# Performance work log

Hardware: AMD Instinct MI355X
Metric: run time of the kernel (lower is better)

## Reference

```python
import jax, jax.numpy as jnp
import numpy as np


def setup_inputs() -> dict:
    key = jax.random.key(0)
    k1, k2 = jax.random.split(key)
    B, N = 2, 8192
    pred = jax.random.normal(k1, (B, N, 3), dtype=jnp.float32)
    gt = jax.random.normal(k2, (B, N, 3), dtype=jnp.float32)
    return {"pred": pred, "gt": gt}


def reference(pred, gt):
    # dist[b, i, j] = ||pred[b, j] - gt[b, i]||_2  (matches torch expand layout:
    # expanded_pred[b,i,j] = pred[b,j], expanded_gt[b,i,j] = gt[b,i]).
    # Computed via the squared-norm expansion to avoid the [B,N,N,3] tensor.
    g2 = jnp.sum(gt * gt, axis=-1)[:, :, None]        # [B, N, 1]
    p2 = jnp.sum(pred * pred, axis=-1)[:, None, :]    # [B, 1, N]
    cross = jnp.einsum('bid,bjd->bij', gt, pred)      # [B, N, N]
    dist = jnp.sqrt(jnp.maximum(g2 + p2 - 2.0 * cross, 0.0))  # [B, N, N]
    dist1 = jnp.min(dist, axis=2)  # min over pred for each gt point
    dist2 = jnp.min(dist, axis=1)  # min over gt for each pred point
    return jnp.mean(jnp.mean(dist1, axis=1) + jnp.mean(dist2, axis=1))
```

## Files before the change

### kernel.cpp

```cpp
#include <hip/hip_runtime.h>
#include <math.h>


#define TILE 1024

__global__ __launch_bounds__(256) void chamfer_partial(
    const float* __restrict__ pred, const float* __restrict__ gt,
    float* __restrict__ ws_max, int N, int B, int S) {
  __shared__ float4 sb[TILE];
  const int tid = threadIdx.x;
  const int z   = blockIdx.z;
  const int dir = z / B;
  const int b   = z - dir * B;
  const float* qbase = (dir == 0) ? gt   : pred;
  const float* obase = (dir == 0) ? pred : gt;

  const int q = blockIdx.x * blockDim.x + tid;
  const float qx = qbase[(size_t)(b * N + q) * 3 + 0];
  const float qy = qbase[(size_t)(b * N + q) * 3 + 1];
  const float qz = qbase[(size_t)(b * N + q) * 3 + 2];

  const int chunk = N / S;
  const int start = blockIdx.y * chunk;

  float m0 = -INFINITY, m1 = -INFINITY, m2 = -INFINITY, m3 = -INFINITY;

  for (int t0 = 0; t0 < chunk; t0 += TILE) {
    for (int p = tid; p < TILE; p += blockDim.x) {
      const float* src = &obase[(size_t)(b * N + start + t0 + p) * 3];
      const float x = src[0], y = src[1], zc = src[2];
      sb[p] = make_float4(x, y, zc, -0.5f * (x * x + y * y + zc * zc));
    }
    __syncthreads();
    #pragma unroll 2
    for (int k = 0; k < TILE; k += 4) {
      const float4 p0 = sb[k + 0];
      const float4 p1 = sb[k + 1];
      const float4 p2 = sb[k + 2];
      const float4 p3 = sb[k + 3];
      m0 = fmaxf(m0, fmaf(qx, p0.x, fmaf(qy, p0.y, fmaf(qz, p0.z, p0.w))));
      m1 = fmaxf(m1, fmaf(qx, p1.x, fmaf(qy, p1.y, fmaf(qz, p1.z, p1.w))));
      m2 = fmaxf(m2, fmaf(qx, p2.x, fmaf(qy, p2.y, fmaf(qz, p2.z, p2.w))));
      m3 = fmaxf(m3, fmaf(qx, p3.x, fmaf(qy, p3.y, fmaf(qz, p3.z, p3.w))));
    }
    __syncthreads();
  }
  const float m = fmaxf(fmaxf(m0, m1), fmaxf(m2, m3));
  ws_max[((size_t)z * N + q) * S + blockIdx.y] = m;
}

__global__ __launch_bounds__(256) void chamfer_combine(
    const float* __restrict__ pred, const float* __restrict__ gt,
    const float* __restrict__ ws_max, float* __restrict__ out,
    int N, int B, int S, float scale) {
  const int idx = blockIdx.x * blockDim.x + threadIdx.x;
  const int z   = idx / N;
  const int q   = idx - z * N;
  const int dir = z / B;
  const int b   = z - dir * B;
  const float* qbase = (dir == 0) ? gt : pred;

  const float qx = qbase[(size_t)(b * N + q) * 3 + 0];
  const float qy = qbase[(size_t)(b * N + q) * 3 + 1];
  const float qz = qbase[(size_t)(b * N + q) * 3 + 2];
  const float g2 = qx * qx + qy * qy + qz * qz;

  const float* wp = &ws_max[((size_t)z * N + q) * S];
  float m = wp[0];
  for (int s = 1; s < S; ++s) m = fmaxf(m, wp[s]);

  float v = sqrtf(fmaxf(g2 - 2.0f * m, 0.0f));

  for (int off = 32; off > 0; off >>= 1) v += __shfl_down(v, off);
  __shared__ float wsum[4];
  const int wid = threadIdx.x >> 6, lane = threadIdx.x & 63;
  if (lane == 0) wsum[wid] = v;
  __syncthreads();
  if (threadIdx.x == 0) {
    const float s4 = wsum[0] + wsum[1] + wsum[2] + wsum[3];
    atomicAdd(out, s4 * scale);
  }
}

extern "C" void kernel_launch(void* const* d_in, const int* in_sizes, int n_in,
                              void* d_out, int out_size, void* d_ws, size_t ws_size,
                              hipStream_t stream) {
  const float* pred = (const float*)d_in[0];
  const float* gt   = (const float*)d_in[1];
  float* out = (float*)d_out;

  const int B = 2;
  const int N = in_sizes[0] / (B * 3);

  int S = 8;
  size_t need = (size_t)2 * B * N * S * sizeof(float);
  while (S > 1 && need > ws_size) { S >>= 1; need >>= 1; }
  float* ws_max = (float*)d_ws;

  hipMemsetAsync(d_out, 0, sizeof(float), stream);

  dim3 g1(N / 256, S, 2 * B);
  chamfer_partial<<<g1, 256, 0, stream>>>(pred, gt, ws_max, N, B, S);

  const int total = 2 * B * N;
  chamfer_combine<<<total / 256, 256, 0, stream>>>(
      pred, gt, ws_max, out, N, B, S, 1.0f / (float)(B * N));
}
```

Baseline: 92.86 us.

## Register-block 8 queries per thread and split reference set into 64 chunks

Each thread now holds 8 query points in registers, so every float4 read from LDS is reused across 8 FMA chains instead of one. The reference set is split into 64 chunks of 128 points, with one shared-memory fill and a single barrier per block. The partial-max workspace is transposed to a [z][chunk][N] layout so the combine kernel reads coalesced. The workspace-size fallback is removed, which assumes ws holds 64 partials per query and drops the previous guard against a small workspace.

```diff
diff --git a/kernel.cpp b/kernel.cpp
--- a/kernel.cpp
+++ b/kernel.cpp
@@ -2,72 +2,70 @@
 #include <math.h>
 
 
-#define TILE 1024
+#define S_CHUNKS 64
+#define Q_PER_T  8
+#define CHUNK    128
 
 __global__ __launch_bounds__(256) void chamfer_partial(
     const float* __restrict__ pred, const float* __restrict__ gt,
-    float* __restrict__ ws_max, int N, int B, int S) {
-  __shared__ float4 sb[TILE];
+    float* __restrict__ ws_max, int N) {
+  __shared__ float4 sb[CHUNK];
   const int tid = threadIdx.x;
   const int z   = blockIdx.z;
-  const int dir = z / B;
-  const int b   = z - dir * B;
-  const float* qbase = (dir == 0) ? gt   : pred;
-  const float* obase = (dir == 0) ? pred : gt;
+  const int dir = z >> 1, b = z & 1;
+  const float* qb = dir ? pred : gt;
+  const float* ob = dir ? gt : pred;
+  const int s = blockIdx.y;
 
-  const int q = blockIdx.x * blockDim.x + tid;
-  const float qx = qbase[(size_t)(b * N + q) * 3 + 0];
-  const float qy = qbase[(size_t)(b * N + q) * 3 + 1];
-  const float qz = qbase[(size_t)(b * N + q) * 3 + 2];
+  if (tid < CHUNK) {
+    const float* src = &ob[(size_t)(b * N + s * CHUNK + tid) * 3];
+    const float x = src[0], y = src[1], zz = src[2];
+    sb[tid] = make_float4(x, y, zz, -0.5f * (x * x + y * y + zz * zz));
+  }
 
-  const int chunk = N / S;
-  const int start = blockIdx.y * chunk;
+  const int q0 = blockIdx.x * (256 * Q_PER_T) + tid;
+  float qx[Q_PER_T], qy[Q_PER_T], qz[Q_PER_T], acc[Q_PER_T];
+  #pragma unroll
+  for (int k = 0; k < Q_PER_T; ++k) {
+    const float* src = &qb[(size_t)(b * N + q0 + k * 256) * 3];
+    qx[k] = src[0]; qy[k] = src[1]; qz[k] = src[2];
+    acc[k] = -INFINITY;
+  }
+  __syncthreads();
 
-  float m0 = -INFINITY, m1 = -INFINITY, m2 = -INFINITY, m3 = -INFINITY;
+  #pragma unroll 4
+  for (int p = 0; p < CHUNK; ++p) {
+    const float4 pt = sb[p];
+    #pragma unroll
+    for (int k = 0; k < Q_PER_T; ++k) {
+      acc[k] = fmaxf(acc[k],
+                     fmaf(qx[k], pt.x, fmaf(qy[k], pt.y, fmaf(qz[k], pt.z, pt.w))));
+    }
+  }
 
-  for (int t0 = 0; t0 < chunk; t0 += TILE) {
-    for (int p = tid; p < TILE; p += blockDim.x) {
-      const float* src = &obase[(size_t)(b * N + start + t0 + p) * 3];
-      const float x = src[0], y = src[1], zc = src[2];
-      sb[p] = make_float4(x, y, zc, -0.5f * (x * x + y * y + zc * zc));
-    }
-    __syncthreads();
-    #pragma unroll 2
-    for (int k = 0; k < TILE; k += 4) {
-      const float4 p0 = sb[k + 0];
-      const float4 p1 = sb[k + 1];
-      const float4 p2 = sb[k + 2];
-      const float4 p3 = sb[k + 3];
-      m0 = fmaxf(m0, fmaf(qx, p0.x, fmaf(qy, p0.y, fmaf(qz, p0.z, p0.w))));
-      m1 = fmaxf(m1, fmaf(qx, p1.x, fmaf(qy, p1.y, fmaf(qz, p1.z, p1.w))));
-      m2 = fmaxf(m2, fmaf(qx, p2.x, fmaf(qy, p2.y, fmaf(qz, p2.z, p2.w))));
-      m3 = fmaxf(m3, fmaf(qx, p3.x, fmaf(qy, p3.y, fmaf(qz, p3.z, p3.w))));
-    }
-    __syncthreads();
-  }
-  const float m = fmaxf(fmaxf(m0, m1), fmaxf(m2, m3));
-  ws_max[((size_t)z * N + q) * S + blockIdx.y] = m;
+  #pragma unroll
+  for (int k = 0; k < Q_PER_T; ++k)
+    ws_max[((size_t)(z * S_CHUNKS + s)) * N + q0 + k * 256] = acc[k];
 }
 
 __global__ __launch_bounds__(256) void chamfer_combine(
     const float* __restrict__ pred, const float* __restrict__ gt,
     const float* __restrict__ ws_max, float* __restrict__ out,
-    int N, int B, int S, float scale) {
+    int N, float scale) {
   const int idx = blockIdx.x * blockDim.x + threadIdx.x;
   const int z   = idx / N;
   const int q   = idx - z * N;
-  const int dir = z / B;
-  const int b   = z - dir * B;
-  const float* qbase = (dir == 0) ? gt : pred;
+  const int dir = z >> 1, b = z & 1;
+  const float* qb = dir ? pred : gt;
 
-  const float qx = qbase[(size_t)(b * N + q) * 3 + 0];
-  const float qy = qbase[(size_t)(b * N + q) * 3 + 1];
-  const float qz = qbase[(size_t)(b * N + q) * 3 + 2];
-  const float g2 = qx * qx + qy * qy + qz * qz;
+  const float* src = &qb[(size_t)(b * N + q) * 3];
+  const float x = src[0], y = src[1], zz = src[2];
+  const float g2 = x * x + y * y + zz * zz;
 
-  const float* wp = &ws_max[((size_t)z * N + q) * S];
-  float m = wp[0];
-  for (int s = 1; s < S; ++s) m = fmaxf(m, wp[s]);
+  float m = -INFINITY;
+  #pragma unroll
+  for (int s = 0; s < S_CHUNKS; ++s)
+    m = fmaxf(m, ws_max[((size_t)(z * S_CHUNKS + s)) * N + q]);
 
   float v = sqrtf(fmaxf(g2 - 2.0f * m, 0.0f));
 
@@ -77,8 +75,7 @@
   if (lane == 0) wsum[wid] = v;
   __syncthreads();
   if (threadIdx.x == 0) {
-    const float s4 = wsum[0] + wsum[1] + wsum[2] + wsum[3];
-    atomicAdd(out, s4 * scale);
+    atomicAdd(out, (wsum[0] + wsum[1] + wsum[2] + wsum[3]) * scale);
   }
 }
 
@@ -91,18 +88,14 @@
 
   const int B = 2;
   const int N = in_sizes[0] / (B * 3);
-
-  int S = 8;
-  size_t need = (size_t)2 * B * N * S * sizeof(float);
-  while (S > 1 && need > ws_size) { S >>= 1; need >>= 1; }
   float* ws_max = (float*)d_ws;
 
   hipMemsetAsync(d_out, 0, sizeof(float), stream);
 
-  dim3 g1(N / 256, S, 2 * B);
-  chamfer_partial<<<g1, 256, 0, stream>>>(pred, gt, ws_max, N, B, S);
+  dim3 g1(N / (256 * Q_PER_T), S_CHUNKS, 2 * B);
+  chamfer_partial<<<g1, 256, 0, stream>>>(pred, gt, ws_max, N);
 
   const int total = 2 * B * N;
   chamfer_combine<<<total / 256, 256, 0, stream>>>(
-      pred, gt, ws_max, out, N, B, S, 1.0f / (float)(B * N));
+      pred, gt, ws_max, out, N, 1.0f / (float)(B * N));
 }
```

After: 89.41 us. 1.04x faster.
